# Optimization experiments

Measured on AMD Instinct MI355X. Metric: run time of the kernel, lower is better.

The kernel has to match this reference:

```python
import jax, jax.numpy as jnp
import numpy as np

N_NODES = 100000
N_EDGES = 3200000
N_GRAPHS = 512
F_IN = 128
HID = 256
N_LABELS = 10


def setup_inputs() -> dict:
    key = jax.random.key(0)
    ks = jax.random.split(key, 16)
    x = jax.random.normal(ks[0], (N_NODES, F_IN), dtype=jnp.float32)
    edge_index = jax.random.randint(ks[1], (2, N_EDGES), 0, N_NODES)
    batch = jnp.sort(jax.random.randint(ks[2], (N_NODES,), 0, N_GRAPHS))
    dims = [(F_IN, HID), (HID, HID), (HID, HID), (HID, HID // 2), (HID // 2, HID // 2), (HID // 2, HID // 4)]
    inp = {"x": x, "edge_index": edge_index, "batch": batch, "primary_idxs_in_batch": 0}
    for i, (di, do) in enumerate(dims, 1):
        inp[f"W{i}"] = jax.random.normal(ks[2 + i], (di, do), dtype=jnp.float32) * (1.0 / np.sqrt(di))
        inp[f"b{i}"] = jnp.zeros((do,), dtype=jnp.float32)
    inp["Wlin"] = jax.random.normal(ks[12], (HID // 4, N_LABELS), dtype=jnp.float32) * (1.0 / np.sqrt(HID // 4))
    inp["blin"] = jnp.zeros((N_LABELS,), dtype=jnp.float32)
    return inp


def _gcn_conv(h, W, b, src, dst, norm):
    # dense transform first (smaller of the two sides), then normalized scatter-aggregate
    m = (h @ W)[src] * norm[:, None]  # [E+N, C_out]
    return jax.ops.segment_sum(m, dst, num_segments=N_NODES) + b


def reference(x, edge_index, batch, primary_idxs_in_batch,
              W1, b1, W2, b2, W3, b3, W4, b4, W5, b5, W6, b6, Wlin, blin):
    loops = jnp.arange(N_NODES, dtype=edge_index.dtype)
    src = jnp.concatenate([edge_index[0], loops])  # A + I (self loops)
    dst = jnp.concatenate([edge_index[1], loops])
    deg = jax.ops.segment_sum(jnp.ones_like(dst, dtype=x.dtype), dst, num_segments=N_NODES)
    dinv = jnp.where(deg > 0, jax.lax.rsqrt(deg), 0.0)
    norm = dinv[src] * dinv[dst]  # D^-1/2 (A+I) D^-1/2 edge weights

    h = jax.nn.relu(_gcn_conv(x, W1, b1, src, dst, norm))
    h = jax.nn.relu(_gcn_conv(h, W2, b2, src, dst, norm))
    h = jax.nn.relu(_gcn_conv(h, W3, b3, src, dst, norm))
    h = jax.nn.relu(_gcn_conv(h, W4, b4, src, dst, norm))
    h = jax.nn.relu(_gcn_conv(h, W5, b5, src, dst, norm))
    h = _gcn_conv(h, W6, b6, src, dst, norm)

    # primary_idxs_in_batch is falsy (0) -> global_mean_pool path
    s = jax.ops.segment_sum(h, batch, num_segments=N_GRAPHS)
    cnt = jax.ops.segment_sum(jnp.ones((N_NODES,), dtype=h.dtype), batch, num_segments=N_GRAPHS)
    pooled = s / jnp.maximum(cnt, 1.0)[:, None]  # [G, HID//4]

    logits = pooled @ Wlin + blin  # [G, labels]
    return (jax.nn.log_softmax(logits, axis=1), jax.nn.softmax(logits, axis=1))
```

## Files before the change

kernel.cpp:

```cpp
#include <hip/hip_runtime.h>
#include <math.h>

#define NN 100000
#define NE 3200000
#define NG 512
#define SB 98
#define NBK 784
#define EBLK 782
#define NWIN 13

typedef __attribute__((ext_vector_type(8))) short short8;
typedef __attribute__((ext_vector_type(4))) float f32x4;
typedef __attribute__((ext_vector_type(2))) float f32x2;

__device__ __forceinline__ float bf2f(unsigned short h){
  return __uint_as_float(((unsigned int)h) << 16);
}
__device__ __forceinline__ unsigned short f2bf(float f){
  unsigned int u = __float_as_uint(f);
  unsigned int r = (u + 0x7fffu + ((u >> 16) & 1u)) >> 16;
  return (unsigned short)r;
}
__device__ __forceinline__ void unpack16(uint4 v, float* f){
  f32x2 p;
  p = __builtin_amdgcn_cvt_pk_f32_fp8(v.x, 0); f[0]=p[0];  f[1]=p[1];
  p = __builtin_amdgcn_cvt_pk_f32_fp8(v.x, 1); f[2]=p[0];  f[3]=p[1];
  p = __builtin_amdgcn_cvt_pk_f32_fp8(v.y, 0); f[4]=p[0];  f[5]=p[1];
  p = __builtin_amdgcn_cvt_pk_f32_fp8(v.y, 1); f[6]=p[0];  f[7]=p[1];
  p = __builtin_amdgcn_cvt_pk_f32_fp8(v.z, 0); f[8]=p[0];  f[9]=p[1];
  p = __builtin_amdgcn_cvt_pk_f32_fp8(v.z, 1); f[10]=p[0]; f[11]=p[1];
  p = __builtin_amdgcn_cvt_pk_f32_fp8(v.w, 0); f[12]=p[0]; f[13]=p[1];
  p = __builtin_amdgcn_cvt_pk_f32_fp8(v.w, 1); f[14]=p[0]; f[15]=p[1];
}
__device__ __forceinline__ unsigned char f2fp8(float v){
  int p = __builtin_amdgcn_cvt_pk_fp8_f32(v, v, 0, 0);
  return (unsigned char)p;
}

__global__ __launch_bounds__(256) void hist2_k(const int* __restrict__ ei,
    int* __restrict__ cnt, int* __restrict__ btot){
  __shared__ int lh[NBK];
  int t = threadIdx.x, b = blockIdx.x;
  for (int i=t; i<NBK; i+=256) lh[i] = 0;
  __syncthreads();
  int base = b*4096;
  #pragma unroll
  for (int u=0; u<16; u++){
    int e = base + u*256 + t;
    if (e < NE) atomicAdd(&lh[ei[NE + e] >> 7], 1);
  }
  __syncthreads();
  for (int i=t; i<NBK; i+=256){
    int v = lh[i];
    cnt[b*NBK + i] = v;
    if (v) atomicAdd(&btot[i], v);
  }
}
__global__ void bscan2_k(const int* __restrict__ btot, int* __restrict__ bptr){
  __shared__ int sc[1024];
  int t = threadIdx.x;
  int v = (t < NBK) ? btot[t] : 0;
  sc[t] = v; __syncthreads();
  for (int off=1; off<1024; off<<=1){
    int u = (t>=off) ? sc[t-off] : 0;
    __syncthreads(); sc[t] += u; __syncthreads();
  }
  if (t < NBK) bptr[t] = sc[t] - v;
  if (t == 1023) bptr[NBK] = sc[1023];
}
__global__ __launch_bounds__(256) void bkpfx_k(int* __restrict__ cnt, const int* __restrict__ bptr){
  __shared__ int sc[256];
  int b = blockIdx.x, t = threadIdx.x;
  int carry = bptr[b];
  for (int base=0; base<EBLK; base+=256){
    int blk = base + t;
    int v = (blk < EBLK) ? cnt[blk*NBK + b] : 0;
    sc[t] = v; __syncthreads();
    for (int off=1; off<256; off<<=1){
      int u = (t>=off) ? sc[t-off] : 0;
      __syncthreads(); sc[t] += u; __syncthreads();
    }
    if (blk < EBLK) cnt[blk*NBK + b] = carry + sc[t] - v;
    carry += sc[255];
    __syncthreads();
  }
}
__global__ __launch_bounds__(256) void scat2_k(const int* __restrict__ ei,
    const int* __restrict__ cnt, uint2* __restrict__ ebuf){
  __shared__ int lh[NBK];
  __shared__ int lo[NBK];
  int t = threadIdx.x, b = blockIdx.x;
  for (int i=t; i<NBK; i+=256){ lh[i] = 0; lo[i] = cnt[b*NBK + i]; }
  __syncthreads();
  int base = b*4096;
  #pragma unroll
  for (int u=0; u<16; u++){
    int e = base + u*256 + t;
    if (e < NE){
      int s = ei[e], d = ei[NE + e];
      int bk = d >> 7;
      int r = atomicAdd(&lh[bk], 1);
      ebuf[lo[bk] + r] = make_uint2((unsigned)s, (unsigned)d);
    }
  }
}
__global__ __launch_bounds__(256) void bdeg_k(const uint2* __restrict__ ebuf,
    const int* __restrict__ bptr, int* __restrict__ deg){
  __shared__ int cnt[128];
  int b = blockIdx.x, t = threadIdx.x;
  if (t < 128) cnt[t] = 0;
  __syncthreads();
  int beg = bptr[b], end = bptr[b+1];
  int nbase = b << 7;
  for (int e = beg + t; e < end; e += 256)
    atomicAdd(&cnt[(int)ebuf[e].y - nbase], 1);
  __syncthreads();
  if (t < 128){
    int node = nbase + t;
    if (node < NN) deg[node] = cnt[t];
  }
}
__global__ __launch_bounds__(256) void ccol_k(const uint2* __restrict__ ebuf,
    const int* __restrict__ bptr, const int* __restrict__ rp, int* __restrict__ col){
  __shared__ int rpl[128];
  __shared__ int cur[128];
  int b = blockIdx.x, t = threadIdx.x;
  int nbase = b << 7;
  if (t < 128){
    int node = nbase + t;
    rpl[t] = (node < NN) ? rp[node] : 0;
    cur[t] = 0;
  }
  __syncthreads();
  int beg = bptr[b], end = bptr[b+1];
  for (int w = 0; w < NWIN; w++){
    for (int e = beg + t; e < end; e += 256){
      uint2 sd = ebuf[e];
      if ((int)(sd.x >> 13) == w){
        int li = (int)sd.y - nbase;
        int pos = rpl[li] + atomicAdd(&cur[li], 1);
        col[pos] = (int)sd.x;
      }
    }
    __syncthreads();
  }
}

__global__ void scanA_k(const int* __restrict__ deg, int* __restrict__ bsum){
  __shared__ int red[256];
  int b = blockIdx.x, t = threadIdx.x;
  int base = b*1024 + t*4;
  int s = 0;
  #pragma unroll
  for (int u=0;u<4;u++){ int i = base+u; s += (i < NN) ? deg[i] : 0; }
  red[t] = s; __syncthreads();
  for (int off=128; off>0; off>>=1){
    if (t < off) red[t] += red[t+off];
    __syncthreads();
  }
  if (t==0) bsum[b] = red[0];
}
__global__ void scanB_k(int* __restrict__ bsum, int* __restrict__ rp){
  __shared__ int sc[128];
  int t = threadIdx.x;
  int v = (t < SB) ? bsum[t] : 0;
  sc[t] = v; __syncthreads();
  for (int off=1; off<128; off<<=1){
    int u = (t>=off) ? sc[t-off] : 0;
    __syncthreads(); sc[t] += u; __syncthreads();
  }
  if (t < SB) bsum[t] = sc[t] - v;
  if (t == 127) rp[NN] = sc[127];
}
__global__ void scanC_k(const int* __restrict__ deg, const int* __restrict__ bsum,
                        int* __restrict__ rp, float* __restrict__ dinv){
  __shared__ int sc[256];
  int b = blockIdx.x, t = threadIdx.x;
  int base = b*1024 + t*4;
  int d[4]; int s = 0;
  #pragma unroll
  for (int u=0;u<4;u++){ int i = base+u; d[u] = (i < NN) ? deg[i] : 0; s += d[u]; }
  sc[t] = s; __syncthreads();
  for (int off=1; off<256; off<<=1){
    int u = (t>=off) ? sc[t-off] : 0;
    __syncthreads(); sc[t] += u; __syncthreads();
  }
  int run = bsum[b] + sc[t] - s;
  #pragma unroll
  for (int u=0;u<4;u++){
    int i = base+u;
    if (i < NN){ rp[i] = run; dinv[i] = rsqrtf((float)(d[u] + 1)); }
    run += d[u];
  }
}

__global__ void f2q_k(const float* __restrict__ in, unsigned char* __restrict__ out, int n4){
  int i = blockIdx.x*256 + threadIdx.x;
  if (i < n4){
    float4 v = ((const float4*)in)[i];
    int p = __builtin_amdgcn_cvt_pk_fp8_f32(v.x, v.y, 0, 0);
    p = __builtin_amdgcn_cvt_pk_fp8_f32(v.z, v.w, p, 1);
    ((unsigned int*)out)[i] = (unsigned int)p;
  }
}
__global__ void wswz_all_k(const float* W1, const float* W2, const float* W3,
                           const float* W4, const float* W5, const float* W6,
                           unsigned short* O1, unsigned short* O2, unsigned short* O3,
                           unsigned short* O4, unsigned short* O5, unsigned short* O6){
  int cfg = blockIdx.y;
  int K, N; const float* W; unsigned short* out;
  switch(cfg){
    case 0: K=128; N=256; W=W1; out=O1; break;
    case 1: K=256; N=256; W=W2; out=O2; break;
    case 2: K=256; N=256; W=W3; out=O3; break;
    case 3: K=256; N=128; W=W4; out=O4; break;
    case 4: K=128; N=128; W=W5; out=O5; break;
    default:K=128; N=64;  W=W6; out=O6; break;
  }
  int idx = blockIdx.x*256 + threadIdx.x;
  int total = K*N/8;
  if (idx >= total) return;
  int l = idx & 15;
  int t = idx >> 4; int q = t & 3; t >>= 2;
  int NT = N/16;
  int nt = t % NT, kt = t / NT;
  int kbase = kt*32 + q*8, n = nt*16 + l;
  short8 o;
  #pragma unroll
  for (int j=0;j<8;j++) o[j] = (short)f2bf(W[(size_t)(kbase+j)*N + n]);
  *(short8*)(out + (size_t)idx*8) = o;
}

template<int C, bool SRC_SCALE, bool RELU, bool HAS_BIAS>
__global__ __launch_bounds__(256) void spmm8_k(const unsigned char* __restrict__ in,
    unsigned short* __restrict__ out,
    const int* __restrict__ rp, const int* __restrict__ col,
    const float* __restrict__ dinv, const float* __restrict__ bias)
{
  constexpr int LPR = C/16;
  constexpr int RPW = 64/LPR;
  constexpr int RPB = 4*RPW;
  int tid = threadIdx.x;
  int wv = tid >> 6, lane = tid & 63;
  int sub = lane / LPR, li = lane % LPR;
  int row = blockIdx.x*RPB + wv*RPW + sub;
  if (row >= NN) return;
  int beg = rp[row], end = rp[row+1];
  float di = dinv[row];
  int co = li*16;
  const unsigned char* inb = in + co;
  float acc[16], tmp[16];
  unpack16(*(const uint4*)(inb + (size_t)row*C), acc);
  if (SRC_SCALE){
    #pragma unroll
    for (int v=0;v<16;v++) acc[v] *= di;
  }
  int j = beg;
  for (; j+8 <= end; j += 8){
    int s[8]; uint4 v[8]; float wgt[8];
    #pragma unroll
    for (int u=0;u<8;u++) s[u] = col[j+u];
    #pragma unroll
    for (int u=0;u<8;u++) v[u] = *(const uint4*)(inb + (size_t)s[u]*C);
    if (SRC_SCALE){
      #pragma unroll
      for (int u=0;u<8;u++) wgt[u] = dinv[s[u]];
    }
    #pragma unroll
    for (int u=0;u<8;u++){
      unpack16(v[u], tmp);
      float w = SRC_SCALE ? wgt[u] : 1.f;
      #pragma unroll
      for (int vv=0;vv<16;vv++) acc[vv] = fmaf(w, tmp[vv], acc[vv]);
    }
  }
  for (; j < end; j++){
    int ss = col[j];
    uint4 v = *(const uint4*)(inb + (size_t)ss*C);
    float w = SRC_SCALE ? dinv[ss] : 1.f;
    unpack16(v, tmp);
    #pragma unroll
    for (int vv=0;vv<16;vv++) acc[vv] = fmaf(w, tmp[vv], acc[vv]);
  }
  float bb[16];
  if (HAS_BIAS){
    #pragma unroll
    for (int u=0;u<4;u++) *(float4*)&bb[u*4] = *(const float4*)(bias + co + u*4);
  }
  #pragma unroll
  for (int v=0;v<16;v++){
    acc[v] *= di;
    if (HAS_BIAS) acc[v] += bb[v];
    if (RELU) acc[v] = fmaxf(acc[v], 0.f);
  }
  uint4 o0, o1;
  o0.x = (unsigned int)f2bf(acc[0])  | ((unsigned int)f2bf(acc[1])<<16);
  o0.y = (unsigned int)f2bf(acc[2])  | ((unsigned int)f2bf(acc[3])<<16);
  o0.z = (unsigned int)f2bf(acc[4])  | ((unsigned int)f2bf(acc[5])<<16);
  o0.w = (unsigned int)f2bf(acc[6])  | ((unsigned int)f2bf(acc[7])<<16);
  o1.x = (unsigned int)f2bf(acc[8])  | ((unsigned int)f2bf(acc[9])<<16);
  o1.y = (unsigned int)f2bf(acc[10]) | ((unsigned int)f2bf(acc[11])<<16);
  o1.z = (unsigned int)f2bf(acc[12]) | ((unsigned int)f2bf(acc[13])<<16);
  o1.w = (unsigned int)f2bf(acc[14]) | ((unsigned int)f2bf(acc[15])<<16);
  unsigned short* op = out + (size_t)row*C + co;
  *(uint4*)op = o0;
  *(uint4*)(op + 8) = o1;
}

template<int K, int N, int EPI>
__global__ __launch_bounds__(256) void mgemm_k(const unsigned short* __restrict__ A,
    const unsigned short* __restrict__ Bsw,
    const float* __restrict__ aux, unsigned short* __restrict__ Cb,
    unsigned char* __restrict__ Cq, int M)
{
  constexpr int NT = N/16, KT = K/32;
  __shared__ short8 Bl[2][NT*64];
  int tid = threadIdx.x;
  int w = tid >> 6, lane = tid & 63;
  int l = lane & 15, q = lane >> 4;
  int rb = blockIdx.x*128 + w*32;
  int r0 = min(rb + l, M-1);
  int r1 = min(rb + 16 + l, M-1);
  f32x4 acc0[NT], acc1[NT];
  #pragma unroll
  for (int nt=0; nt<NT; nt++){ acc0[nt] = (f32x4){0,0,0,0}; acc1[nt] = (f32x4){0,0,0,0}; }
  const unsigned short* ap0 = A + (size_t)r0*K + q*8;
  const unsigned short* ap1 = A + (size_t)r1*K + q*8;
  const short8* bsrc = (const short8*)Bsw;
  #pragma unroll
  for (int i=0;i<NT/4;i++) Bl[0][i*256 + tid] = bsrc[i*256 + tid];
  for (int kt=0; kt<KT; kt++){
    __syncthreads();
    if (kt+1 < KT){
      const short8* s = bsrc + (size_t)(kt+1)*NT*64;
      #pragma unroll
      for (int i=0;i<NT/4;i++) Bl[(kt+1)&1][i*256 + tid] = s[i*256 + tid];
    }
    short8 a0 = *(const short8*)(ap0 + kt*32);
    short8 a1 = *(const short8*)(ap1 + kt*32);
    const short8* bl = &Bl[kt&1][0];
    #pragma unroll
    for (int nt=0; nt<NT; nt++){
      short8 bf = bl[(nt*4 + q)*16 + l];
      acc0[nt] = __builtin_amdgcn_mfma_f32_16x16x32_bf16(a0, bf, acc0[nt], 0,0,0);
      acc1[nt] = __builtin_amdgcn_mfma_f32_16x16x32_bf16(a1, bf, acc1[nt], 0,0,0);
    }
  }
  #pragma unroll
  for (int half=0; half<2; half++){
    int rbb = rb + half*16;
    #pragma unroll
    for (int nt=0; nt<NT; nt++){
      f32x4 a = half ? acc1[nt] : acc0[nt];
      int n = nt*16 + l;
      #pragma unroll
      for (int r=0;r<4;r++){
        int row = rbb + q*4 + r;
        if (row < M){
          float v = a[r];
          if (EPI == 0){
            v = fmaxf(v + aux[n], 0.f);
            Cb[(size_t)row*N + n] = f2bf(v);
          } else {
            v *= aux[row];
            Cq[(size_t)row*N + n] = f2fp8(v);
          }
        }
      }
    }
  }
}

__global__ __launch_bounds__(256) void poolhead_k(const unsigned short* __restrict__ h,
    const int* __restrict__ batch, const float* __restrict__ Wlin,
    const float* __restrict__ blin, float* __restrict__ out)
{
  __shared__ int range[2];
  __shared__ float red[4][64];
  __shared__ float pl[64];
  int g = blockIdx.x;
  if (threadIdx.x < 2){
    int target = g + threadIdx.x;
    int lo = 0, hi = NN;
    while (lo < hi){ int m = (lo+hi) >> 1; if (batch[m] < target) lo = m+1; else hi = m; }
    range[threadIdx.x] = lo;
  }
  __syncthreads();
  int lo = range[0], hi = range[1];
  int ch = threadIdx.x & 63, rg = threadIdx.x >> 6;
  float s = 0.f;
  for (int r = lo + rg; r < hi; r += 4) s += bf2f(h[(size_t)r*64 + ch]);
  red[rg][ch] = s; __syncthreads();
  if (rg == 0){
    float tot = red[0][ch] + red[1][ch] + red[2][ch] + red[3][ch];
    pl[ch] = tot / fmaxf((float)(hi - lo), 1.f);
  }
  __syncthreads();
  if (threadIdx.x == 0){
    float l[10];
    #pragma unroll
    for (int j=0;j<10;j++) l[j] = blin[j];
    for (int c=0;c<64;c++){
      float p = pl[c];
      #pragma unroll
      for (int j=0;j<10;j++) l[j] = fmaf(p, Wlin[c*10 + j], l[j]);
    }
    float mx = l[0];
    #pragma unroll
    for (int j=1;j<10;j++) mx = fmaxf(mx, l[j]);
    float e[10]; float se = 0.f;
    #pragma unroll
    for (int j=0;j<10;j++){ e[j] = expf(l[j]-mx); se += e[j]; }
    float lse = logf(se);
    #pragma unroll
    for (int j=0;j<10;j++){
      out[g*10 + j]         = l[j] - mx - lse;
      out[NG*10 + g*10 + j] = e[j] / se;
    }
  }
}

extern "C" void kernel_launch(void* const* d_in, const int* in_sizes, int n_in,
                              void* d_out, int out_size, void* d_ws, size_t ws_size,
                              hipStream_t stream)
{
  const float* x     = (const float*)d_in[0];
  const int*   ei    = (const int*)  d_in[1];
  const int*   batch = (const int*)  d_in[2];
  const float* W1=(const float*)d_in[4],  *b1=(const float*)d_in[5];
  const float* W2=(const float*)d_in[6],  *b2=(const float*)d_in[7];
  const float* W3=(const float*)d_in[8],  *b3=(const float*)d_in[9];
  const float* W4=(const float*)d_in[10], *b4=(const float*)d_in[11];
  const float* W5=(const float*)d_in[12], *b5=(const float*)d_in[13];
  const float* W6=(const float*)d_in[14], *b6=(const float*)d_in[15];
  const float* Wl=(const float*)d_in[16], *bl=(const float*)d_in[17];
  float* out = (float*)d_out;

  char* ws = (char*)d_ws;
  unsigned short* hA  = (unsigned short*)(ws + 0);
  unsigned short* hB  = (unsigned short*)(ws + 51200000);
  unsigned char*  hQ  = (unsigned char*) (ws + 102400000);
  unsigned char*  xq  = (unsigned char*) (ws + 128000000);
  int*   col   = (int*)  (ws + 140800000);
  uint2* ebuf  = (uint2*)(ws + 153600000);
  int*   rp    = (int*)  (ws + 179200000);
  int*   deg   = (int*)  (ws + 179600016);
  float* dinv  = (float*)(ws + 180000016);
  unsigned short* W1s = (unsigned short*)(ws + 180400016);
  unsigned short* W2s = (unsigned short*)(ws + 180465552);
  unsigned short* W3s = (unsigned short*)(ws + 180596624);
  unsigned short* W4s = (unsigned short*)(ws + 180727696);
  unsigned short* W5s = (unsigned short*)(ws + 180793232);
  unsigned short* W6s = (unsigned short*)(ws + 180826000);
  int*   bsum  = (int*)  (ws + 180842384);
  int*   btot  = (int*)  (ws + 180842896);
  int*   bptr  = (int*)  (ws + 180846032);
  int*   cnt   = (int*)  (ws + 180849172 + 12);

  hipMemsetAsync(btot, 0, NBK*4, stream);

  hist2_k <<<EBLK, 256, 0, stream>>>(ei, cnt, btot);
  bscan2_k<<<1, 1024, 0, stream>>>(btot, bptr);
  bkpfx_k <<<NBK, 256, 0, stream>>>(cnt, bptr);
  scat2_k <<<EBLK, 256, 0, stream>>>(ei, cnt, ebuf);
  bdeg_k  <<<NBK, 256, 0, stream>>>(ebuf, bptr, deg);
  scanA_k <<<SB, 256, 0, stream>>>(deg, bsum);
  scanB_k <<<1, 128, 0, stream>>>(bsum, rp);
  scanC_k <<<SB, 256, 0, stream>>>(deg, bsum, rp, dinv);
  ccol_k  <<<NBK, 256, 0, stream>>>(ebuf, bptr, rp, col);

  wswz_all_k<<<dim3(32,6), 256, 0, stream>>>(W1,W2,W3,W4,W5,W6, W1s,W2s,W3s,W4s,W5s,W6s);
  f2q_k<<<(NN*128/4 + 255)/256, 256, 0, stream>>>(x, xq, NN*128/4);

  const int SQ256 = (NN + 15)/16, SQ128 = (NN + 31)/32, SQ64 = (NN + 63)/64;
  const int GB2 = (NN + 127)/128;

  spmm8_k<128,true,false,false><<<SQ128,256,0,stream>>>(xq, hA, rp, col, dinv, nullptr);
  mgemm_k<128,256,0><<<GB2,256,0,stream>>>(hA, W1s, b1, hB, nullptr, NN);
  mgemm_k<256,256,1><<<GB2,256,0,stream>>>(hB, W2s, dinv, nullptr, hQ, NN);
  spmm8_k<256,false,true,true><<<SQ256,256,0,stream>>>(hQ, hA, rp, col, dinv, b2);
  mgemm_k<256,256,1><<<GB2,256,0,stream>>>(hA, W3s, dinv, nullptr, hQ, NN);
  spmm8_k<256,false,true,true><<<SQ256,256,0,stream>>>(hQ, hB, rp, col, dinv, b3);
  mgemm_k<256,128,1><<<GB2,256,0,stream>>>(hB, W4s, dinv, nullptr, hQ, NN);
  spmm8_k<128,false,true,true><<<SQ128,256,0,stream>>>(hQ, hA, rp, col, dinv, b4);
  mgemm_k<128,128,1><<<GB2,256,0,stream>>>(hA, W5s, dinv, nullptr, hQ, NN);
  spmm8_k<128,false,true,true><<<SQ128,256,0,stream>>>(hQ, hB, rp, col, dinv, b5);
  mgemm_k<128,64,1><<<GB2,256,0,stream>>>(hB, W6s, dinv, nullptr, hQ, NN);
  spmm8_k<64,false,false,true><<<SQ64,256,0,stream>>>(hQ, hA, rp, col, dinv, b6);

  poolhead_k<<<NG, 256, 0, stream>>>(hA, batch, Wl, bl, out);
}
```

Measured before the change: 1.138 ms.

## Fuse CSR build into one kernel and slice SpMM features per XCD

Five preprocessing kernels (bucket degree count, three-pass global scan, windowed column fill) are merged into one per-bucket kernel. It derives row pointers from the existing bucket offsets with a local 128-entry scan and fills the column array in a single pass. This drops the source-window ordering of column indices, which may hurt gather locality. Separately, the SpMM kernels split the feature dimension into slices assigned by blockIdx mod 8, so each XCD's L2 only caches a fraction of the gathered feature rows. The cost is more rows per block and more blocks overall.

```diff
diff --git a/kernel.cpp b/kernel.cpp
--- a/kernel.cpp
+++ b/kernel.cpp
@@ -4,10 +4,8 @@
 #define NN 100000
 #define NE 3200000
 #define NG 512
-#define SB 98
-#define NBK 784
+#define NBK 782
 #define EBLK 782
-#define NWIN 13
 
 typedef __attribute__((ext_vector_type(8))) short short8;
 typedef __attribute__((ext_vector_type(4))) float f32x4;
@@ -104,93 +102,46 @@
     }
   }
 }
-__global__ __launch_bounds__(256) void bdeg_k(const uint2* __restrict__ ebuf,
-    const int* __restrict__ bptr, int* __restrict__ deg){
+__global__ __launch_bounds__(256) void bcsr_k(const uint2* __restrict__ ebuf,
+    const int* __restrict__ bptr, int* __restrict__ rp, float* __restrict__ dinv,
+    int* __restrict__ col){
   __shared__ int cnt[128];
+  __shared__ int off[128];
+  __shared__ int sc[128];
   int b = blockIdx.x, t = threadIdx.x;
+  int nbase = b << 7;
+  int beg = bptr[b], end = bptr[b+1];
   if (t < 128) cnt[t] = 0;
   __syncthreads();
-  int beg = bptr[b], end = bptr[b+1];
-  int nbase = b << 7;
   for (int e = beg + t; e < end; e += 256)
     atomicAdd(&cnt[(int)ebuf[e].y - nbase], 1);
   __syncthreads();
+  int v = (t < 128) ? cnt[t] : 0;
+  if (t < 128) sc[t] = v;
+  __syncthreads();
+  for (int o2=1; o2<128; o2<<=1){
+    int u = (t < 128 && t >= o2) ? sc[t-o2] : 0;
+    __syncthreads();
+    if (t < 128) sc[t] += u;
+    __syncthreads();
+  }
   if (t < 128){
     int node = nbase + t;
-    if (node < NN) deg[node] = cnt[t];
-  }
-}
-__global__ __launch_bounds__(256) void ccol_k(const uint2* __restrict__ ebuf,
-    const int* __restrict__ bptr, const int* __restrict__ rp, int* __restrict__ col){
-  __shared__ int rpl[128];
-  __shared__ int cur[128];
-  int b = blockIdx.x, t = threadIdx.x;
-  int nbase = b << 7;
-  if (t < 128){
-    int node = nbase + t;
-    rpl[t] = (node < NN) ? rp[node] : 0;
-    cur[t] = 0;
-  }
-  __syncthreads();
-  int beg = bptr[b], end = bptr[b+1];
-  for (int w = 0; w < NWIN; w++){
-    for (int e = beg + t; e < end; e += 256){
-      uint2 sd = ebuf[e];
-      if ((int)(sd.x >> 13) == w){
-        int li = (int)sd.y - nbase;
-        int pos = rpl[li] + atomicAdd(&cur[li], 1);
-        col[pos] = (int)sd.x;
-      }
-    }
-    __syncthreads();
-  }
-}
-
-__global__ void scanA_k(const int* __restrict__ deg, int* __restrict__ bsum){
-  __shared__ int red[256];
-  int b = blockIdx.x, t = threadIdx.x;
-  int base = b*1024 + t*4;
-  int s = 0;
-  #pragma unroll
-  for (int u=0;u<4;u++){ int i = base+u; s += (i < NN) ? deg[i] : 0; }
-  red[t] = s; __syncthreads();
-  for (int off=128; off>0; off>>=1){
-    if (t < off) red[t] += red[t+off];
-    __syncthreads();
-  }
-  if (t==0) bsum[b] = red[0];
-}
-__global__ void scanB_k(int* __restrict__ bsum, int* __restrict__ rp){
-  __shared__ int sc[128];
-  int t = threadIdx.x;
-  int v = (t < SB) ? bsum[t] : 0;
-  sc[t] = v; __syncthreads();
-  for (int off=1; off<128; off<<=1){
-    int u = (t>=off) ? sc[t-off] : 0;
-    __syncthreads(); sc[t] += u; __syncthreads();
-  }
-  if (t < SB) bsum[t] = sc[t] - v;
-  if (t == 127) rp[NN] = sc[127];
-}
-__global__ void scanC_k(const int* __restrict__ deg, const int* __restrict__ bsum,
-                        int* __restrict__ rp, float* __restrict__ dinv){
-  __shared__ int sc[256];
-  int b = blockIdx.x, t = threadIdx.x;
-  int base = b*1024 + t*4;
-  int d[4]; int s = 0;
-  #pragma unroll
-  for (int u=0;u<4;u++){ int i = base+u; d[u] = (i < NN) ? deg[i] : 0; s += d[u]; }
-  sc[t] = s; __syncthreads();
-  for (int off=1; off<256; off<<=1){
-    int u = (t>=off) ? sc[t-off] : 0;
-    __syncthreads(); sc[t] += u; __syncthreads();
-  }
-  int run = bsum[b] + sc[t] - s;
-  #pragma unroll
-  for (int u=0;u<4;u++){
-    int i = base+u;
-    if (i < NN){ rp[i] = run; dinv[i] = rsqrtf((float)(d[u] + 1)); }
-    run += d[u];
+    if (node < NN){
+      int ex = beg + sc[t] - v;
+      rp[node] = ex;
+      off[t] = ex;
+      dinv[node] = rsqrtf((float)(v + 1));
+      cnt[t] = 0;
+    }
+  }
+  if (b == ((NN-1) >> 7) && t == 0) rp[NN] = end;
+  __syncthreads();
+  for (int e = beg + t; e < end; e += 256){
+    uint2 sd = ebuf[e];
+    int li = (int)sd.y - nbase;
+    int pos = off[li] + atomicAdd(&cnt[li], 1);
+    col[pos] = (int)sd.x;
   }
 }
 
@@ -231,23 +182,32 @@
   *(short8*)(out + (size_t)idx*8) = o;
 }
 
-template<int C, bool SRC_SCALE, bool RELU, bool HAS_BIAS>
-__global__ __launch_bounds__(256) void spmm8_k(const unsigned char* __restrict__ in,
+template<int C, int SLICES, bool SRC_SCALE, bool RELU, bool HAS_BIAS>
+__global__ __launch_bounds__(256) void spmms_k(const unsigned char* __restrict__ in,
     unsigned short* __restrict__ out,
     const int* __restrict__ rp, const int* __restrict__ col,
     const float* __restrict__ dinv, const float* __restrict__ bias)
 {
-  constexpr int LPR = C/16;
-  constexpr int RPW = 64/LPR;
-  constexpr int RPB = 4*RPW;
+  constexpr int CS  = C / SLICES;
+  constexpr int LPR = CS / 16;
+  constexpr int RPW = 64 / LPR;
+  constexpr int RPB = 4 * RPW;
+  constexpr int XPG = 8 / SLICES;
+  constexpr int NRB = (NN + RPB - 1) / RPB;
+  int bx = blockIdx.x;
+  int xcd = bx & 7;
+  int slice = xcd % SLICES;
+  int part  = xcd / SLICES;
+  int rb = (bx >> 3) * XPG + part;
+  if (rb >= NRB) return;
   int tid = threadIdx.x;
   int wv = tid >> 6, lane = tid & 63;
   int sub = lane / LPR, li = lane % LPR;
-  int row = blockIdx.x*RPB + wv*RPW + sub;
+  int row = rb*RPB + wv*RPW + sub;
   if (row >= NN) return;
   int beg = rp[row], end = rp[row+1];
   float di = dinv[row];
-  int co = li*16;
+  int co = slice*CS + li*16;
   const unsigned char* inb = in + co;
   float acc[16], tmp[16];
   unpack16(*(const uint4*)(inb + (size_t)row*C), acc);
@@ -444,7 +404,6 @@
   int*   col   = (int*)  (ws + 140800000);
   uint2* ebuf  = (uint2*)(ws + 153600000);
   int*   rp    = (int*)  (ws + 179200000);
-  int*   deg   = (int*)  (ws + 179600016);
   float* dinv  = (float*)(ws + 180000016);
   unsigned short* W1s = (unsigned short*)(ws + 180400016);
   unsigned short* W2s = (unsigned short*)(ws + 180465552);
@@ -452,10 +411,9 @@
   unsigned short* W4s = (unsigned short*)(ws + 180727696);
   unsigned short* W5s = (unsigned short*)(ws + 180793232);
   unsigned short* W6s = (unsigned short*)(ws + 180826000);
-  int*   bsum  = (int*)  (ws + 180842384);
   int*   btot  = (int*)  (ws + 180842896);
   int*   bptr  = (int*)  (ws + 180846032);
-  int*   cnt   = (int*)  (ws + 180849172 + 12);
+  int*   cnt   = (int*)  (ws + 180849184);
 
   hipMemsetAsync(btot, 0, NBK*4, stream);
 
@@ -463,30 +421,29 @@
   bscan2_k<<<1, 1024, 0, stream>>>(btot, bptr);
   bkpfx_k <<<NBK, 256, 0, stream>>>(cnt, bptr);
   scat2_k <<<EBLK, 256, 0, stream>>>(ei, cnt, ebuf);
-  bdeg_k  <<<NBK, 256, 0, stream>>>(ebuf, bptr, deg);
-  scanA_k <<<SB, 256, 0, stream>>>(deg, bsum);
-  scanB_k <<<1, 128, 0, stream>>>(bsum, rp);
-  scanC_k <<<SB, 256, 0, stream>>>(deg, bsum, rp, dinv);
-  ccol_k  <<<NBK, 256, 0, stream>>>(ebuf, bptr, rp, col);
+  bcsr_k  <<<NBK, 256, 0, stream>>>(ebuf, bptr, rp, dinv, col);
 
   wswz_all_k<<<dim3(32,6), 256, 0, stream>>>(W1,W2,W3,W4,W5,W6, W1s,W2s,W3s,W4s,W5s,W6s);
   f2q_k<<<(NN*128/4 + 255)/256, 256, 0, stream>>>(x, xq, NN*128/4);
 
-  const int SQ256 = (NN + 15)/16, SQ128 = (NN + 31)/32, SQ64 = (NN + 63)/64;
+  const int NRB = (NN + 63)/64;
+  const int G4 = 8 * ((NRB + 1)/2);
+  const int G2 = 8 * ((NRB + 3)/4);
+  const int G1 = 8 * ((NRB + 7)/8);
   const int GB2 = (NN + 127)/128;
 
-  spmm8_k<128,true,false,false><<<SQ128,256,0,stream>>>(xq, hA, rp, col, dinv, nullptr);
+  spmms_k<128,2,true,false,false><<<G2,256,0,stream>>>(xq, hA, rp, col, dinv, nullptr);
   mgemm_k<128,256,0><<<GB2,256,0,stream>>>(hA, W1s, b1, hB, nullptr, NN);
   mgemm_k<256,256,1><<<GB2,256,0,stream>>>(hB, W2s, dinv, nullptr, hQ, NN);
-  spmm8_k<256,false,true,true><<<SQ256,256,0,stream>>>(hQ, hA, rp, col, dinv, b2);
+  spmms_k<256,4,false,true,true><<<G4,256,0,stream>>>(hQ, hA, rp, col, dinv, b2);
   mgemm_k<256,256,1><<<GB2,256,0,stream>>>(hA, W3s, dinv, nullptr, hQ, NN);
-  spmm8_k<256,false,true,true><<<SQ256,256,0,stream>>>(hQ, hB, rp, col, dinv, b3);
+  spmms_k<256,4,false,true,true><<<G4,256,0,stream>>>(hQ, hB, rp, col, dinv, b3);
   mgemm_k<256,128,1><<<GB2,256,0,stream>>>(hB, W4s, dinv, nullptr, hQ, NN);
-  spmm8_k<128,false,true,true><<<SQ128,256,0,stream>>>(hQ, hA, rp, col, dinv, b4);
+  spmms_k<128,2,false,true,true><<<G2,256,0,stream>>>(hQ, hA, rp, col, dinv, b4);
   mgemm_k<128,128,1><<<GB2,256,0,stream>>>(hA, W5s, dinv, nullptr, hQ, NN);
-  spmm8_k<128,false,true,true><<<SQ128,256,0,stream>>>(hQ, hB, rp, col, dinv, b5);
+  spmms_k<128,2,false,true,true><<<G2,256,0,stream>>>(hQ, hB, rp, col, dinv, b5);
   mgemm_k<128,64,1><<<GB2,256,0,stream>>>(hB, W6s, dinv, nullptr, hQ, NN);
-  spmm8_k<64,false,false,true><<<SQ64,256,0,stream>>>(hQ, hA, rp, col, dinv, b6);
+  spmms_k<64,1,false,false,true><<<G1,256,0,stream>>>(hQ, hA, rp, col, dinv, b6);
 
   poolhead_k<<<NG, 256, 0, stream>>>(hA, batch, Wl, bl, out);
 }
```

After: 1.387 ms. 21.9% more time.
